# Performance work log

Hardware: AMD Instinct MI355X
Metric: run time of the kernel (lower is better)

The kernel has to match this reference:

```python
import jax, jax.numpy as jnp
import numpy as np

# fp4 e2m1 representable magnitudes and round-to-nearest midpoints
_FP4_LEVELS = jnp.array([0.0, 0.5, 1.0, 1.5, 2.0, 3.0, 4.0, 6.0], dtype=jnp.float32)
_FP4_MIDS = jnp.array([0.25, 0.75, 1.25, 1.75, 2.5, 3.5, 5.0], dtype=jnp.float32)


def fp4_get_scalar(x):
    return jnp.mean(jnp.abs(x))


def fp4_quant_dequant(x, s):
    # quant(x, s) then rquant(x, s): round x/s to nearest fp4e2m1 value, scale back
    y = x / s
    idx = jnp.searchsorted(_FP4_MIDS, jnp.abs(y), side='right')
    q = jnp.sign(y) * _FP4_LEVELS[idx]
    return q * s


def setup_inputs() -> dict:
    key = jax.random.key(0)
    k1, k2, k3 = jax.random.split(key, 3)
    B, S, IN, OUT = 4, 2048, 4096, 4096
    input = jax.random.normal(k1, (B, S, IN), dtype=jnp.float32)
    # kaiming-uniform-ish weight, small bias
    bound_w = np.sqrt(6.0 / IN) / np.sqrt(1 + 5.0)
    weight = jax.random.uniform(k2, (OUT, IN), minval=-bound_w, maxval=bound_w, dtype=jnp.float32)
    bound_b = 1.0 / np.sqrt(IN)
    bias = jax.random.uniform(k3, (OUT,), minval=-bound_b, maxval=bound_b, dtype=jnp.float32)
    return {"input": input, "weight": weight, "bias": bias}


def reference(input, weight, bias):
    q_scalar = 1.0
    input_scalar = fp4_get_scalar(input) * q_scalar
    weight_scalar = fp4_get_scalar(weight) * q_scalar
    x_q = fp4_quant_dequant(input, input_scalar)      # [B,S,IN]
    w_q = fp4_quant_dequant(weight, weight_scalar)    # [OUT,IN]
    out = jnp.einsum('bsi,oi->bso', x_q, w_q) + bias  # [B,S,OUT]
    return out
```

## Files before the change

kernel.cpp:

```cpp
#include <hip/hip_runtime.h>
#include <hip/hip_bf16.h>
#include <stdint.h>

typedef __attribute__((ext_vector_type(16))) float f32x16;
typedef __attribute__((ext_vector_type(8))) int i32x8;

#define M_DIM 8192
#define N_DIM 4096
#define K_DIM 4096
#define NX_INV (1.0f / 33554432.0f)
#define NW_INV (1.0f / 16777216.0f)

__global__ void absum2_kernel(const float* __restrict__ x, const float* __restrict__ w,
                              double* __restrict__ sums) {
    bool isw = blockIdx.x >= 2048;
    const float4* src = (const float4*)(isw ? w : x);
    int n4  = isw ? (16777216 / 4) : (33554432 / 4);
    int bid = isw ? (blockIdx.x - 2048) : blockIdx.x;
    int nb  = isw ? 1024 : 2048;
    int i = bid * blockDim.x + threadIdx.x;
    int stride = nb * blockDim.x;
    float s = 0.f;
    for (; i < n4; i += stride) {
        float4 v = src[i];
        s += fabsf(v.x) + fabsf(v.y) + fabsf(v.z) + fabsf(v.w);
    }
    #pragma unroll
    for (int off = 32; off >= 1; off >>= 1) s += __shfl_down(s, off, 64);
    __shared__ float wsum[4];
    int lane = threadIdx.x & 63, wid = threadIdx.x >> 6;
    if (lane == 0) wsum[wid] = s;
    __syncthreads();
    if (threadIdx.x == 0) {
        double tot = (double)wsum[0] + (double)wsum[1] + (double)wsum[2] + (double)wsum[3];
        atomicAdd(&sums[isw ? 1 : 0], tot);
    }
}

__device__ __forceinline__ uint32_t enc_nib_t(float x, float t0, float t1, float t2,
                                              float t3, float t4, float t5, float t6) {
    float a = fabsf(x);
    uint32_t idx;
    if (a < t3) idx = (a < t1) ? ((a < t0) ? 0u : 1u) : ((a < t2) ? 2u : 3u);
    else        idx = (a < t5) ? ((a < t4) ? 4u : 5u) : ((a < t6) ? 6u : 7u);
    return idx | ((__float_as_uint(x) >> 31) << 3);
}

__global__ void quant2_kernel(const float* __restrict__ X, const float* __restrict__ W,
                              uint32_t* __restrict__ Xp, uint32_t* __restrict__ Wp,
                              const double* __restrict__ sums) {
    __shared__ float4 tile[32 * 64];

    bool isw = blockIdx.x >= 4096;
    const float* src_base = isw ? W : X;
    uint32_t* dst = isw ? Wp : Xp;
    float s = (float)(sums[isw ? 1 : 0]) * (isw ? NW_INV : NX_INV);
    int bid = isw ? (blockIdx.x - 4096) : blockIdx.x;

    float t0 = 0.25f * s, t1 = 0.75f * s, t2 = 1.25f * s, t3 = 1.75f * s;
    float t4 = 2.5f * s,  t5 = 3.5f * s,  t6 = 5.0f * s;

    int mb  = bid >> 4;
    int ktg = bid & 15;
    int t = threadIdx.x;

    {
        int row0 = t >> 6;
        int col4 = t & 63;
        const float4* src = (const float4*)(src_base + (size_t)(mb * 32 + row0) * K_DIM + ktg * 256) + col4;
        #pragma unroll
        for (int p = 0; p < 8; p++) {
            int row = p * 4 + row0;
            tile[row * 64 + (col4 ^ (row & 7))] = src[(size_t)p * 4 * (K_DIM / 4)];
        }
    }
    __syncthreads();

    int w = t >> 6;
    int l = t & 63;
    int row = l & 31;
    int ub = w * 16 + (l >> 5) * 8;
    uint32_t o[4];
    #pragma unroll
    for (int d = 0; d < 4; d++) {
        float4 f0 = tile[row * 64 + ((ub + 2 * d)     ^ (row & 7))];
        float4 f1 = tile[row * 64 + ((ub + 2 * d + 1) ^ (row & 7))];
        o[d] =  enc_nib_t(f0.x, t0,t1,t2,t3,t4,t5,t6)
             | (enc_nib_t(f0.y, t0,t1,t2,t3,t4,t5,t6) << 4)
             | (enc_nib_t(f0.z, t0,t1,t2,t3,t4,t5,t6) << 8)
             | (enc_nib_t(f0.w, t0,t1,t2,t3,t4,t5,t6) << 12)
             | (enc_nib_t(f1.x, t0,t1,t2,t3,t4,t5,t6) << 16)
             | (enc_nib_t(f1.y, t0,t1,t2,t3,t4,t5,t6) << 20)
             | (enc_nib_t(f1.z, t0,t1,t2,t3,t4,t5,t6) << 24)
             | (enc_nib_t(f1.w, t0,t1,t2,t3,t4,t5,t6) << 28);
    }
    int kt = ktg * 4 + w;
    *(uint4*)(dst + ((size_t)(mb * 64 + kt) * 64 + l) * 4) = make_uint4(o[0], o[1], o[2], o[3]);
}

#define NWG 512

__device__ __forceinline__ i32x8 dupfrag(uint4 u) {
    i32x8 v;
    v[0] = u.x; v[1] = u.y; v[2] = u.z; v[3] = u.w;
    v[4] = u.x; v[5] = u.y; v[6] = u.z; v[7] = u.w;
    return v;
}

#define LOADST(S, kt) do {                                      \
    S##a0 = *(const uint4*)(pA0 + (size_t)(kt) * 256);          \
    S##a1 = *(const uint4*)(pA1 + (size_t)(kt) * 256);          \
    S##a2 = *(const uint4*)(pA2 + (size_t)(kt) * 256);          \
    S##a3 = *(const uint4*)(pA3 + (size_t)(kt) * 256);          \
    S##b0 = *(const uint4*)(pB0 + (size_t)(kt) * 256);          \
    S##b1 = *(const uint4*)(pB1 + (size_t)(kt) * 256);          \
    S##b2 = *(const uint4*)(pB2 + (size_t)(kt) * 256);          \
    S##b3 = *(const uint4*)(pB3 + (size_t)(kt) * 256);          \
} while (0)

#define MFMA_ROW(VA, B0, B1, B2, B3, C0, C1, C2, C3) do {                         \
    i32x8 va_ = dupfrag(VA);                                                      \
    C0 = __builtin_amdgcn_mfma_scale_f32_32x32x64_f8f6f4(va_, B0, C0, 4, 4, 0, 0x7F7F7F7F, 0, 0x7F7F7F7F); \
    C1 = __builtin_amdgcn_mfma_scale_f32_32x32x64_f8f6f4(va_, B1, C1, 4, 4, 0, 0x7F7F7F7F, 0, 0x7F7F7F7F); \
    C2 = __builtin_amdgcn_mfma_scale_f32_32x32x64_f8f6f4(va_, B2, C2, 4, 4, 0, 0x7F7F7F7F, 0, 0x7F7F7F7F); \
    C3 = __builtin_amdgcn_mfma_scale_f32_32x32x64_f8f6f4(va_, B3, C3, 4, 4, 0, 0x7F7F7F7F, 0, 0x7F7F7F7F); \
} while (0)

#define MFMA_TILE(S) do {                                                         \
    i32x8 vb0_ = dupfrag(S##b0), vb1_ = dupfrag(S##b1);                           \
    i32x8 vb2_ = dupfrag(S##b2), vb3_ = dupfrag(S##b3);                           \
    __builtin_amdgcn_s_setprio(1);                                                \
    MFMA_ROW(S##a0, vb0_, vb1_, vb2_, vb3_, acc00, acc01, acc02, acc03);          \
    MFMA_ROW(S##a1, vb0_, vb1_, vb2_, vb3_, acc10, acc11, acc12, acc13);          \
    MFMA_ROW(S##a2, vb0_, vb1_, vb2_, vb3_, acc20, acc21, acc22, acc23);          \
    MFMA_ROW(S##a3, vb0_, vb1_, vb2_, vb3_, acc30, acc31, acc32, acc33);          \
    __builtin_amdgcn_s_setprio(0);                                                \
} while (0)

#define EPI(ACC, MM, NN) do {                                                     \
    int col_ = colb + (NN) * 32;                                                  \
    float bv_ = bias[col_];                                                       \
    _Pragma("unroll")                                                             \
    for (int i = 0; i < 16; i++) {                                                \
        int row_ = rowb + (MM) * 32 + (i & 3) + ((i >> 2) << 3);                  \
        __builtin_nontemporal_store(ACC[i] * scale + bv_,                         \
                                    &C[(size_t)row_ * N_DIM + col_]);             \
    }                                                                             \
} while (0)

__global__ __launch_bounds__(256, 1)
void gemm_kernel(const uint32_t* __restrict__ Ap, const uint32_t* __restrict__ Bp,
                 const float* __restrict__ bias, float* __restrict__ C,
                 const double* __restrict__ sums) {
    int bid = blockIdx.x;
    int swz = (bid & 7) * 64 + (bid >> 3);
    int bm = (swz >> 4) * 256;
    int bn = (swz & 15) * 256;

    int lane = threadIdx.x & 63;
    int wid = threadIdx.x >> 6;
    int wm = wid >> 1;
    int wn = wid & 1;

    const uint32_t* pA0 = Ap + (size_t)((bm >> 5) + wm * 4 + 0) * 16384 + lane * 4;
    const uint32_t* pA1 = Ap + (size_t)((bm >> 5) + wm * 4 + 1) * 16384 + lane * 4;
    const uint32_t* pA2 = Ap + (size_t)((bm >> 5) + wm * 4 + 2) * 16384 + lane * 4;
    const uint32_t* pA3 = Ap + (size_t)((bm >> 5) + wm * 4 + 3) * 16384 + lane * 4;
    const uint32_t* pB0 = Bp + (size_t)((bn >> 5) + wn * 4 + 0) * 16384 + lane * 4;
    const uint32_t* pB1 = Bp + (size_t)((bn >> 5) + wn * 4 + 1) * 16384 + lane * 4;
    const uint32_t* pB2 = Bp + (size_t)((bn >> 5) + wn * 4 + 2) * 16384 + lane * 4;
    const uint32_t* pB3 = Bp + (size_t)((bn >> 5) + wn * 4 + 3) * 16384 + lane * 4;

    f32x16 acc00 = (f32x16)0.f, acc01 = (f32x16)0.f, acc02 = (f32x16)0.f, acc03 = (f32x16)0.f;
    f32x16 acc10 = (f32x16)0.f, acc11 = (f32x16)0.f, acc12 = (f32x16)0.f, acc13 = (f32x16)0.f;
    f32x16 acc20 = (f32x16)0.f, acc21 = (f32x16)0.f, acc22 = (f32x16)0.f, acc23 = (f32x16)0.f;
    f32x16 acc30 = (f32x16)0.f, acc31 = (f32x16)0.f, acc32 = (f32x16)0.f, acc33 = (f32x16)0.f;

    uint4 S0a0, S0a1, S0a2, S0a3, S0b0, S0b1, S0b2, S0b3;
    uint4 S1a0, S1a1, S1a2, S1a3, S1b0, S1b1, S1b2, S1b3;
    uint4 S2a0, S2a1, S2a2, S2a3, S2b0, S2b1, S2b2, S2b3;

    LOADST(S0, 0);
    LOADST(S1, 1);
    LOADST(S2, 2);
    for (int kt = 0; kt < 63; kt += 3) {
        MFMA_TILE(S0);
        if (kt + 3 < 64) LOADST(S0, kt + 3);
        MFMA_TILE(S1);
        if (kt + 4 < 64) LOADST(S1, kt + 4);
        MFMA_TILE(S2);
        if (kt + 5 < 64) LOADST(S2, kt + 5);
    }
    MFMA_TILE(S0);

    float scale = (float)((sums[0] * (1.0 / 33554432.0)) * (sums[1] * (1.0 / 16777216.0)));

    int colb = bn + wn * 128 + (lane & 31);
    int rowb = bm + wm * 128 + ((lane >> 5) << 2);
    EPI(acc00, 0, 0); EPI(acc01, 0, 1); EPI(acc02, 0, 2); EPI(acc03, 0, 3);
    EPI(acc10, 1, 0); EPI(acc11, 1, 1); EPI(acc12, 1, 2); EPI(acc13, 1, 3);
    EPI(acc20, 2, 0); EPI(acc21, 2, 1); EPI(acc22, 2, 2); EPI(acc23, 2, 3);
    EPI(acc30, 3, 0); EPI(acc31, 3, 1); EPI(acc32, 3, 2); EPI(acc33, 3, 3);
}

extern "C" void kernel_launch(void* const* d_in, const int* in_sizes, int n_in,
                              void* d_out, int out_size, void* d_ws, size_t ws_size,
                              hipStream_t stream) {
    const float* x    = (const float*)d_in[0];
    const float* w    = (const float*)d_in[1];
    const float* bias = (const float*)d_in[2];
    float* out = (float*)d_out;

    double* sums = (double*)d_ws;
    uint32_t* Xp = (uint32_t*)((char*)d_ws + 1024);
    uint32_t* Wp = Xp + (size_t)256 * 64 * 64 * 4;

    hipMemsetAsync(d_ws, 0, 1024, stream);
    absum2_kernel<<<3072, 256, 0, stream>>>(x, w, sums);
    quant2_kernel<<<6144, 256, 0, stream>>>(x, w, Xp, Wp, sums);
    gemm_kernel<<<NWG, 256, 0, stream>>>(Xp, Wp, bias, out, sums);
}
```

Before: 183.9 us.

## Split GEMM workgroup into eight waves with 128x64 subtiles and double buffering

The GEMM block grows from 4 to 8 waves (512 threads, launch bounds 512,2). Each wave now computes a 128x64 subtile with 8 accumulators instead of 16, and the register pipeline drops from triple to double buffering. This lowers per-wave register pressure so more waves fit per CU and hide latency better. In exchange each wave reuses its A loads less, so A is fetched from global memory twice as often per block, and the prefetch distance is shorter.

New measurement: 192.4 us. +4.6%, slower.

```diff
diff --git a/kernel.cpp b/kernel.cpp
--- a/kernel.cpp
+++ b/kernel.cpp
@@ -114,26 +114,21 @@
     S##a3 = *(const uint4*)(pA3 + (size_t)(kt) * 256);          \
     S##b0 = *(const uint4*)(pB0 + (size_t)(kt) * 256);          \
     S##b1 = *(const uint4*)(pB1 + (size_t)(kt) * 256);          \
-    S##b2 = *(const uint4*)(pB2 + (size_t)(kt) * 256);          \
-    S##b3 = *(const uint4*)(pB3 + (size_t)(kt) * 256);          \
-} while (0)
-
-#define MFMA_ROW(VA, B0, B1, B2, B3, C0, C1, C2, C3) do {                         \
+} while (0)
+
+#define MFMA_ROW2(VA, B0, B1, C0, C1) do {                                        \
     i32x8 va_ = dupfrag(VA);                                                      \
     C0 = __builtin_amdgcn_mfma_scale_f32_32x32x64_f8f6f4(va_, B0, C0, 4, 4, 0, 0x7F7F7F7F, 0, 0x7F7F7F7F); \
     C1 = __builtin_amdgcn_mfma_scale_f32_32x32x64_f8f6f4(va_, B1, C1, 4, 4, 0, 0x7F7F7F7F, 0, 0x7F7F7F7F); \
-    C2 = __builtin_amdgcn_mfma_scale_f32_32x32x64_f8f6f4(va_, B2, C2, 4, 4, 0, 0x7F7F7F7F, 0, 0x7F7F7F7F); \
-    C3 = __builtin_amdgcn_mfma_scale_f32_32x32x64_f8f6f4(va_, B3, C3, 4, 4, 0, 0x7F7F7F7F, 0, 0x7F7F7F7F); \
 } while (0)
 
 #define MFMA_TILE(S) do {                                                         \
     i32x8 vb0_ = dupfrag(S##b0), vb1_ = dupfrag(S##b1);                           \
-    i32x8 vb2_ = dupfrag(S##b2), vb3_ = dupfrag(S##b3);                           \
     __builtin_amdgcn_s_setprio(1);                                                \
-    MFMA_ROW(S##a0, vb0_, vb1_, vb2_, vb3_, acc00, acc01, acc02, acc03);          \
-    MFMA_ROW(S##a1, vb0_, vb1_, vb2_, vb3_, acc10, acc11, acc12, acc13);          \
-    MFMA_ROW(S##a2, vb0_, vb1_, vb2_, vb3_, acc20, acc21, acc22, acc23);          \
-    MFMA_ROW(S##a3, vb0_, vb1_, vb2_, vb3_, acc30, acc31, acc32, acc33);          \
+    MFMA_ROW2(S##a0, vb0_, vb1_, acc00, acc01);                                   \
+    MFMA_ROW2(S##a1, vb0_, vb1_, acc10, acc11);                                   \
+    MFMA_ROW2(S##a2, vb0_, vb1_, acc20, acc21);                                   \
+    MFMA_ROW2(S##a3, vb0_, vb1_, acc30, acc31);                                   \
     __builtin_amdgcn_s_setprio(0);                                                \
 } while (0)
 
@@ -148,7 +143,7 @@
     }                                                                             \
 } while (0)
 
-__global__ __launch_bounds__(256, 1)
+__global__ __launch_bounds__(512, 2)
 void gemm_kernel(const uint32_t* __restrict__ Ap, const uint32_t* __restrict__ Bp,
                  const float* __restrict__ bias, float* __restrict__ C,
                  const double* __restrict__ sums) {
@@ -159,48 +154,41 @@
 
     int lane = threadIdx.x & 63;
     int wid = threadIdx.x >> 6;
-    int wm = wid >> 1;
-    int wn = wid & 1;
+    int wm = wid >> 2;
+    int wn = wid & 3;
 
     const uint32_t* pA0 = Ap + (size_t)((bm >> 5) + wm * 4 + 0) * 16384 + lane * 4;
     const uint32_t* pA1 = Ap + (size_t)((bm >> 5) + wm * 4 + 1) * 16384 + lane * 4;
     const uint32_t* pA2 = Ap + (size_t)((bm >> 5) + wm * 4 + 2) * 16384 + lane * 4;
     const uint32_t* pA3 = Ap + (size_t)((bm >> 5) + wm * 4 + 3) * 16384 + lane * 4;
-    const uint32_t* pB0 = Bp + (size_t)((bn >> 5) + wn * 4 + 0) * 16384 + lane * 4;
-    const uint32_t* pB1 = Bp + (size_t)((bn >> 5) + wn * 4 + 1) * 16384 + lane * 4;
-    const uint32_t* pB2 = Bp + (size_t)((bn >> 5) + wn * 4 + 2) * 16384 + lane * 4;
-    const uint32_t* pB3 = Bp + (size_t)((bn >> 5) + wn * 4 + 3) * 16384 + lane * 4;
-
-    f32x16 acc00 = (f32x16)0.f, acc01 = (f32x16)0.f, acc02 = (f32x16)0.f, acc03 = (f32x16)0.f;
-    f32x16 acc10 = (f32x16)0.f, acc11 = (f32x16)0.f, acc12 = (f32x16)0.f, acc13 = (f32x16)0.f;
-    f32x16 acc20 = (f32x16)0.f, acc21 = (f32x16)0.f, acc22 = (f32x16)0.f, acc23 = (f32x16)0.f;
-    f32x16 acc30 = (f32x16)0.f, acc31 = (f32x16)0.f, acc32 = (f32x16)0.f, acc33 = (f32x16)0.f;
-
-    uint4 S0a0, S0a1, S0a2, S0a3, S0b0, S0b1, S0b2, S0b3;
-    uint4 S1a0, S1a1, S1a2, S1a3, S1b0, S1b1, S1b2, S1b3;
-    uint4 S2a0, S2a1, S2a2, S2a3, S2b0, S2b1, S2b2, S2b3;
+    const uint32_t* pB0 = Bp + (size_t)((bn >> 5) + wn * 2 + 0) * 16384 + lane * 4;
+    const uint32_t* pB1 = Bp + (size_t)((bn >> 5) + wn * 2 + 1) * 16384 + lane * 4;
+
+    f32x16 acc00 = (f32x16)0.f, acc01 = (f32x16)0.f;
+    f32x16 acc10 = (f32x16)0.f, acc11 = (f32x16)0.f;
+    f32x16 acc20 = (f32x16)0.f, acc21 = (f32x16)0.f;
+    f32x16 acc30 = (f32x16)0.f, acc31 = (f32x16)0.f;
+
+    uint4 S0a0, S0a1, S0a2, S0a3, S0b0, S0b1;
+    uint4 S1a0, S1a1, S1a2, S1a3, S1b0, S1b1;
 
     LOADST(S0, 0);
     LOADST(S1, 1);
-    LOADST(S2, 2);
-    for (int kt = 0; kt < 63; kt += 3) {
+    for (int kt = 0; kt < 64; kt += 2) {
         MFMA_TILE(S0);
-        if (kt + 3 < 64) LOADST(S0, kt + 3);
+        if (kt + 2 < 64) LOADST(S0, kt + 2);
         MFMA_TILE(S1);
-        if (kt + 4 < 64) LOADST(S1, kt + 4);
-        MFMA_TILE(S2);
-        if (kt + 5 < 64) LOADST(S2, kt + 5);
-    }
-    MFMA_TILE(S0);
+        if (kt + 3 < 64) LOADST(S1, kt + 3);
+    }
 
     float scale = (float)((sums[0] * (1.0 / 33554432.0)) * (sums[1] * (1.0 / 16777216.0)));
 
-    int colb = bn + wn * 128 + (lane & 31);
+    int colb = bn + wn * 64 + (lane & 31);
     int rowb = bm + wm * 128 + ((lane >> 5) << 2);
-    EPI(acc00, 0, 0); EPI(acc01, 0, 1); EPI(acc02, 0, 2); EPI(acc03, 0, 3);
-    EPI(acc10, 1, 0); EPI(acc11, 1, 1); EPI(acc12, 1, 2); EPI(acc13, 1, 3);
-    EPI(acc20, 2, 0); EPI(acc21, 2, 1); EPI(acc22, 2, 2); EPI(acc23, 2, 3);
-    EPI(acc30, 3, 0); EPI(acc31, 3, 1); EPI(acc32, 3, 2); EPI(acc33, 3, 3);
+    EPI(acc00, 0, 0); EPI(acc01, 0, 1);
+    EPI(acc10, 1, 0); EPI(acc11, 1, 1);
+    EPI(acc20, 2, 0); EPI(acc21, 2, 1);
+    EPI(acc30, 3, 0); EPI(acc31, 3, 1);
 }
 
 extern "C" void kernel_launch(void* const* d_in, const int* in_sizes, int n_in,
@@ -218,5 +206,5 @@
     hipMemsetAsync(d_ws, 0, 1024, stream);
     absum2_kernel<<<3072, 256, 0, stream>>>(x, w, sums);
     quant2_kernel<<<6144, 256, 0, stream>>>(x, w, Xp, Wp, sums);
-    gemm_kernel<<<NWG, 256, 0, stream>>>(Xp, Wp, bias, out, sums);
-}
+    gemm_kernel<<<NWG, 512, 0, stream>>>(Xp, Wp, bias, out, sums);
+}
```
